# Performance work log

Hardware: AMD Instinct MI355X
Metric: run time of the kernel (lower is better)

The kernel has to match this reference:

```python
import jax, jax.numpy as jnp
import numpy as np

HEAD_SIZE = 128
NUM_EMBED = 1024
BLOCK_SIZE = 2048


def setup_inputs() -> dict:
    key = jax.random.key(0)
    kx, kk, kq, kv = jax.random.split(key, 4)
    x = jax.random.normal(kx, (4, BLOCK_SIZE, NUM_EMBED), dtype=jnp.float32)
    s = 1.0 / np.sqrt(NUM_EMBED)
    Wk = jax.random.normal(kk, (NUM_EMBED, HEAD_SIZE), dtype=jnp.float32) * s
    Wq = jax.random.normal(kq, (NUM_EMBED, HEAD_SIZE), dtype=jnp.float32) * s
    Wv = jax.random.normal(kv, (NUM_EMBED, HEAD_SIZE), dtype=jnp.float32) * s
    return {"x": x, "Wk": Wk, "Wq": Wq, "Wv": Wv}


def reference(x, Wk, Wq, Wv):
    # x: [B, T, C]; W*: [C, H]
    B, T, C = x.shape
    k = x @ Wk          # [B, T, H]
    q = x @ Wq          # [B, T, H]
    v = x @ Wv          # [B, T, H]
    scale = k.shape[-1] ** -0.5
    wei = jnp.einsum('bth,bsh->bts', q, k) * scale  # [B, T, T]
    causal = jnp.tril(jnp.ones((T, T), dtype=bool))
    wei = jnp.where(causal, wei, -jnp.inf)
    wei = jax.nn.softmax(wei, axis=-1)
    out = jnp.einsum('bts,bsh->bth', wei, v)        # [B, T, H]
    return out
```

## Files before the change

kernel.cpp:

```cpp
#include <hip/hip_runtime.h>
#include <hip/hip_bf16.h>
#include <math.h>

#define B_ 4
#define T_ 2048
#define C_ 1024
#define H_ 128
#define SCALE 0.088388347648318447f

typedef unsigned short u16;
typedef __bf16 bf16x8 __attribute__((ext_vector_type(8)));
typedef __bf16 bf16x4 __attribute__((ext_vector_type(4)));
typedef float  f32x4  __attribute__((ext_vector_type(4)));
typedef u16    u16x8  __attribute__((ext_vector_type(8)));
typedef u16    u16x4  __attribute__((ext_vector_type(4)));

#define PO_OFF  0u
#define ML_OFF  18874368u
#define WBT_OFF 19169280u
#define QB_OFF  19955712u
#define KB_OFF  22052864u
#define VT_OFF  24150016u

__device__ __forceinline__ u16 f2bf(float f) {
    __hip_bfloat16 h = __float2bfloat16(f);
    return __builtin_bit_cast(u16, h);
}
__device__ __forceinline__ float bf2f(u16 u) {
    unsigned v = (unsigned)u << 16;
    return __builtin_bit_cast(float, v);
}

__device__ __forceinline__ void load_lds16(const void* g, void* l) {
    __builtin_amdgcn_global_load_lds(
        (const __attribute__((address_space(1))) unsigned int*)g,
        (__attribute__((address_space(3))) unsigned int*)l, 16, 0, 0);
}

__global__ __launch_bounds__(256) void convert_w(const float* __restrict__ Wq,
                                                 const float* __restrict__ Wk,
                                                 const float* __restrict__ Wv,
                                                 u16* __restrict__ wbT) {
    const int id = blockIdx.x * 256 + threadIdx.x;
    const int s = id >> 17;
    const int r = id & 131071;
    const int k = r >> 7, n = r & 127;
    const float* W = (s == 0) ? Wq : (s == 1) ? Wk : Wv;
    float v = W[k * 128 + n];
    if (s == 0) v *= SCALE;
    wbT[(s << 17) + (n << 10) + k] = f2bf(v);
}

__global__ __launch_bounds__(256) void gemm_qkv(
    const float* __restrict__ x, const u16* __restrict__ wbT,
    u16* __restrict__ qb, u16* __restrict__ kb, u16* __restrict__ vT)
{
    __shared__ u16 xs[2][2048];
    __shared__ u16 ws[2][8192];

    const int tid = threadIdx.x;
    const int w = tid >> 6, lane = tid & 63, lg = lane >> 4, lr = lane & 15;
    const int wm = w >> 1, wn = w & 1;
    const int s = blockIdx.y;
    const int m0 = blockIdx.x * 32;
    const u16* wsrc = wbT + (s << 17);

    const int xrow = tid >> 3;
    const int xseg = tid & 7;
    const float* xbase = x + (size_t)(m0 + xrow) * C_ + xseg * 8;
    const unsigned xsw = ((unsigned)xrow & 7u) << 4;

    unsigned wro[4], wco[4];
#pragma unroll
    for (int i = 0; i < 4; ++i) {
        const unsigned o = (unsigned)(w * 4 + i) * 1024u + (unsigned)lane * 16u;
        const unsigned o2 = o ^ (((o >> 7) & 7u) << 4);
        wro[i] = o2 >> 7; wco[i] = (o2 & 127u) >> 1;
    }

    f32x4 acc[4] = {};

    {
        const float4 f0 = ((const float4*)xbase)[0], f1 = ((const float4*)xbase)[1];
#pragma unroll
        for (int i = 0; i < 4; ++i)
            load_lds16(wsrc + (size_t)wro[i] * C_ + wco[i], &ws[0][(w * 4 + i) * 512]);
        u16x8 pk;
        pk[0] = f2bf(f0.x); pk[1] = f2bf(f0.y); pk[2] = f2bf(f0.z); pk[3] = f2bf(f0.w);
        pk[4] = f2bf(f1.x); pk[5] = f2bf(f1.y); pk[6] = f2bf(f1.z); pk[7] = f2bf(f1.w);
        *(u16x8*)((char*)xs[0] + xrow * 128 + (((unsigned)xseg * 16) ^ xsw)) = pk;
    }
    __syncthreads();

    int buf = 0;
    for (int k0 = 0; k0 < C_; k0 += 64) {
        const bool pf = (k0 + 64 < C_);
        float4 g0, g1;
        if (pf) {
            const float* xn = xbase + k0 + 64;
            g0 = ((const float4*)xn)[0]; g1 = ((const float4*)xn)[1];
#pragma unroll
            for (int i = 0; i < 4; ++i)
                load_lds16(wsrc + (size_t)wro[i] * C_ + (k0 + 64) + wco[i],
                           &ws[buf ^ 1][(w * 4 + i) * 512]);
        }

        const int arow = wm * 16 + lr;
        const unsigned asw = ((unsigned)arow & 7u) << 4;
#pragma unroll
        for (int kc = 0; kc < 2; ++kc) {
            const unsigned kb_ = (unsigned)(kc * 64 + lg * 16);
            const bf16x8 af = *(const bf16x8*)((const char*)xs[buf] + arow * 128 + (kb_ ^ asw));
            bf16x8 bfr[4];
#pragma unroll
            for (int ni = 0; ni < 4; ++ni) {
                const int n = wn * 64 + ni * 16 + lr;
                bfr[ni] = *(const bf16x8*)((const char*)ws[buf] + n * 128 + (kb_ ^ (((unsigned)n & 7u) << 4)));
            }
#pragma unroll
            for (int ni = 0; ni < 4; ++ni)
                acc[ni] = __builtin_amdgcn_mfma_f32_16x16x32_bf16(af, bfr[ni], acc[ni], 0, 0, 0);
        }

        if (pf) {
            u16x8 pk;
            pk[0] = f2bf(g0.x); pk[1] = f2bf(g0.y); pk[2] = f2bf(g0.z); pk[3] = f2bf(g0.w);
            pk[4] = f2bf(g1.x); pk[5] = f2bf(g1.y); pk[6] = f2bf(g1.z); pk[7] = f2bf(g1.w);
            *(u16x8*)((char*)xs[buf ^ 1] + xrow * 128 + (((unsigned)xseg * 16) ^ xsw)) = pk;
        }
        __syncthreads();
        buf ^= 1;
    }

    if (s < 2) {
        u16* dst = (s == 0) ? qb : kb;
#pragma unroll
        for (int ni = 0; ni < 4; ++ni) {
            const int trow = m0 + wm * 16 + lg * 4;
            const int col = wn * 64 + ni * 16 + lr;
#pragma unroll
            for (int r = 0; r < 4; ++r)
                dst[(size_t)(trow + r) * H_ + col] = f2bf(acc[ni][r]);
        }
    } else {
#pragma unroll
        for (int ni = 0; ni < 4; ++ni) {
            const int trow = m0 + wm * 16 + lg * 4;
            const int bb = trow >> 11, t = trow & 2047;
            const int d = wn * 64 + ni * 16 + lr;
            u16x4 pk;
            pk[0] = f2bf(acc[ni][0]); pk[1] = f2bf(acc[ni][1]);
            pk[2] = f2bf(acc[ni][2]); pk[3] = f2bf(acc[ni][3]);
            *(u16x4*)&vT[((size_t)bb * 128 + d) * 2048 + t] = pk;
        }
    }
}

__global__ __launch_bounds__(256) void attn_split(
    const u16* __restrict__ qb, const u16* __restrict__ kb,
    const u16* __restrict__ vT, u16* __restrict__ po, float* __restrict__ ml)
{
    __shared__ u16 ks[2][4096];
    __shared__ u16 vs[2][128 * 36];

    const int jt = blockIdx.x, sp = blockIdx.y, b = blockIdx.z;
    const int kt0 = sp * 8;
    const int ktend_all = 2 * jt + 2;
    if (kt0 >= ktend_all) return;
    const int kt_end = min(kt0 + 8, ktend_all);

    const int tid = threadIdx.x;
    const int w = tid >> 6, lane = tid & 63, lg = lane >> 4, lr = lane & 15;
    const int qrow_base = jt * 64 + w * 16;

    const u16* kbB = kb + ((size_t)(b << 11)) * H_;
    const u16* vbB = vT + (size_t)b * 128 * 2048;

    unsigned krow[2], kcolb[2];
#pragma unroll
    for (int i = 0; i < 2; ++i) {
        const unsigned o_ = (unsigned)(w * 2 + i) * 1024u + (unsigned)lane * 16u;
        const unsigned o2 = o_ ^ (((o_ >> 8) & 7u) << 4);
        krow[i] = o2 >> 8; kcolb[i] = o2 & 255u;
    }
    int vd[2], vc[2];
#pragma unroll
    for (int i = 0; i < 2; ++i) {
        const int idx = i * 256 + tid;
        vd[i] = idx >> 2; vc[i] = idx & 3;
    }

    const u16* qp = qb + ((size_t)(b << 11) + qrow_base + lr) * H_;
    bf16x8 qf[4];
#pragma unroll
    for (int kc = 0; kc < 4; ++kc)
        qf[kc] = *(const bf16x8*)&qp[kc * 32 + lg * 8];

    u16x8 vr[2];
    {
        const u16* kbase = kbB + (size_t)kt0 * 32 * H_;
#pragma unroll
        for (int i = 0; i < 2; ++i)
            load_lds16((const char*)kbase + krow[i] * 256 + kcolb[i], &ks[0][(w * 2 + i) * 512]);
        const u16* vbase = vbB + (size_t)kt0 * 32;
#pragma unroll
        for (int i = 0; i < 2; ++i)
            vr[i] = *(const u16x8*)&vbase[(size_t)vd[i] * 2048 + vc[i] * 8];
#pragma unroll
        for (int i = 0; i < 2; ++i) {
            char* rb = (char*)vs[0] + vd[i] * 72 + (vc[i] & 2) * 4;
            *(u16x4*)(rb + ((2 * vc[i]) & 3) * 16)     = __builtin_shufflevector(vr[i], vr[i], 0, 1, 2, 3);
            *(u16x4*)(rb + ((2 * vc[i] + 1) & 3) * 16) = __builtin_shufflevector(vr[i], vr[i], 4, 5, 6, 7);
        }
    }
    __syncthreads();

    f32x4 o[8] = {};
    float m_run = -1e30f, l_run = 0.f;
    int cur = 0;

    for (int kt = kt0; kt < kt_end; ++kt) {
        const bool pf = (kt + 1 < kt_end);
        if (pf) {
            const u16* kbase = kbB + (size_t)(kt + 1) * 32 * H_;
#pragma unroll
            for (int i = 0; i < 2; ++i)
                load_lds16((const char*)kbase + krow[i] * 256 + kcolb[i],
                           &ks[cur ^ 1][(w * 2 + i) * 512]);
            const u16* vbase = vbB + (size_t)(kt + 1) * 32;
#pragma unroll
            for (int i = 0; i < 2; ++i)
                vr[i] = *(const u16x8*)&vbase[(size_t)vd[i] * 2048 + vc[i] * 8];
        }

        f32x4 s0 = {0.f, 0.f, 0.f, 0.f}, s1 = {0.f, 0.f, 0.f, 0.f};
        const unsigned swz = ((unsigned)lr & 7u) << 4;
#pragma unroll
        for (int kc = 0; kc < 4; ++kc) {
            const unsigned byte = ((unsigned)(kc * 64 + lg * 16)) ^ swz;
            const bf16x8 kf0 = *(const bf16x8*)((const char*)ks[cur] + lr * 256 + byte);
            const bf16x8 kf1 = *(const bf16x8*)((const char*)ks[cur] + lr * 256 + 4096 + byte);
            s0 = __builtin_amdgcn_mfma_f32_16x16x32_bf16(kf0, qf[kc], s0, 0, 0, 0);
            s1 = __builtin_amdgcn_mfma_f32_16x16x32_bf16(kf1, qf[kc], s1, 0, 0, 0);
        }

        if (kt * 32 + 31 > qrow_base) {
            const int qg = qrow_base + lr;
            const int kvb = kt * 32 + lg * 4;
#pragma unroll
            for (int r = 0; r < 4; ++r) {
                if (kvb + r > qg)      s0[r] = -INFINITY;
                if (kvb + 16 + r > qg) s1[r] = -INFINITY;
            }
        }

        float mt = fmaxf(fmaxf(fmaxf(s0[0], s0[1]), fmaxf(s0[2], s0[3])),
                         fmaxf(fmaxf(s1[0], s1[1]), fmaxf(s1[2], s1[3])));
        mt = fmaxf(mt, __shfl_xor(mt, 16));
        mt = fmaxf(mt, __shfl_xor(mt, 32));
        if (__any(mt > m_run + 8.f)) {
            const float mn = fmaxf(m_run, mt);
            const float f = __expf(m_run - mn);
            const float fb0 = __shfl(f, lg * 4 + 0);
            const float fb1 = __shfl(f, lg * 4 + 1);
            const float fb2 = __shfl(f, lg * 4 + 2);
            const float fb3 = __shfl(f, lg * 4 + 3);
#pragma unroll
            for (int ni = 0; ni < 8; ++ni) {
                o[ni][0] *= fb0; o[ni][1] *= fb1; o[ni][2] *= fb2; o[ni][3] *= fb3;
            }
            l_run *= f;
            m_run = mn;
        }
        const float p0 = __expf(s0[0] - m_run), p1 = __expf(s0[1] - m_run);
        const float p2 = __expf(s0[2] - m_run), p3 = __expf(s0[3] - m_run);
        const float p4 = __expf(s1[0] - m_run), p5 = __expf(s1[1] - m_run);
        const float p6 = __expf(s1[2] - m_run), p7 = __expf(s1[3] - m_run);
        float sum = ((p0 + p1) + (p2 + p3)) + ((p4 + p5) + (p6 + p7));
        sum += __shfl_xor(sum, 16);
        sum += __shfl_xor(sum, 32);
        l_run += sum;

        bf16x8 pa;
        pa[0] = (__bf16)p0; pa[1] = (__bf16)p1; pa[2] = (__bf16)p2; pa[3] = (__bf16)p3;
        pa[4] = (__bf16)p4; pa[5] = (__bf16)p5; pa[6] = (__bf16)p6; pa[7] = (__bf16)p7;

#pragma unroll
        for (int ni = 0; ni < 8; ++ni) {
            const bf16x8 vf = *(const bf16x8*)((const char*)vs[cur] + (ni * 16 + lr) * 72 + lg * 16);
            o[ni] = __builtin_amdgcn_mfma_f32_16x16x32_bf16(pa, vf, o[ni], 0, 0, 0);
        }

        if (pf) {
#pragma unroll
            for (int i = 0; i < 2; ++i) {
                char* rb = (char*)vs[cur ^ 1] + vd[i] * 72 + (vc[i] & 2) * 4;
                *(u16x4*)(rb + ((2 * vc[i]) & 3) * 16)     = __builtin_shufflevector(vr[i], vr[i], 0, 1, 2, 3);
                *(u16x4*)(rb + ((2 * vc[i] + 1) & 3) * 16) = __builtin_shufflevector(vr[i], vr[i], 4, 5, 6, 7);
            }
        }
        __syncthreads();
        cur ^= 1;
    }

    const int a = jt >> 2, b3 = jt & 3;
    const int slot = (a + 1) * (2 * a + b3) + sp;
    u16* pob = po + (size_t)(b * 144 + slot) * 64 * 128;
#pragma unroll
    for (int ni = 0; ni < 8; ++ni) {
        const int col = ni * 16 + lr;
#pragma unroll
        for (int rj = 0; rj < 4; ++rj)
            pob[(w * 16 + lg * 4 + rj) * 128 + col] = f2bf(o[ni][rj]);
    }
    if (lg == 0) {
        float* mlb = ml + (size_t)(b * 144 + slot) * 128;
        mlb[w * 16 + lr] = m_run;
        mlb[64 + w * 16 + lr] = l_run;
    }
}

__global__ __launch_bounds__(256) void attn_combine(
    const u16* __restrict__ po, const float* __restrict__ ml,
    float* __restrict__ out)
{
    const int rid = (blockIdx.x << 3) + (threadIdx.x >> 5);
    const int b = blockIdx.y;
    const int d4 = (threadIdx.x & 31) * 4;
    const int jt = rid >> 6, row = rid & 63;
    const int a = jt >> 2, b3 = jt & 3;
    const int slot0 = (a + 1) * (2 * a + b3);
    const int c = a + 1;

    float M = -INFINITY;
#pragma unroll
    for (int si = 0; si < 8; ++si)
        if (si < c) M = fmaxf(M, ml[(size_t)(b * 144 + slot0 + si) * 128 + row]);

    float L = 0.f;
    float a0 = 0.f, a1 = 0.f, a2 = 0.f, a3 = 0.f;
#pragma unroll
    for (int si = 0; si < 8; ++si) {
        if (si < c) {
            const float* mlb = ml + (size_t)(b * 144 + slot0 + si) * 128;
            const float wgt = __expf(mlb[row] - M);
            L += wgt * mlb[64 + row];
            const u16x4 t = *(const u16x4*)&po[((size_t)(b * 144 + slot0 + si) * 64 + row) * 128 + d4];
            a0 = fmaf(wgt, bf2f(t[0]), a0); a1 = fmaf(wgt, bf2f(t[1]), a1);
            a2 = fmaf(wgt, bf2f(t[2]), a2); a3 = fmaf(wgt, bf2f(t[3]), a3);
        }
    }
    const float inv = 1.f / L;
    *(float4*)&out[((size_t)(b << 11) + rid) * H_ + d4] =
        make_float4(a0 * inv, a1 * inv, a2 * inv, a3 * inv);
}

extern "C" void kernel_launch(void* const* d_in, const int* in_sizes, int n_in,
                              void* d_out, int out_size, void* d_ws, size_t ws_size,
                              hipStream_t stream) {
    const float* x  = (const float*)d_in[0];
    const float* Wk = (const float*)d_in[1];
    const float* Wq = (const float*)d_in[2];
    const float* Wv = (const float*)d_in[3];
    float* out = (float*)d_out;

    u16* po   = (u16*)((char*)d_ws + PO_OFF);
    float* ml = (float*)((char*)d_ws + ML_OFF);
    u16* wbT  = (u16*)((char*)d_ws + WBT_OFF);
    u16* qb   = (u16*)((char*)d_ws + QB_OFF);
    u16* kb   = (u16*)((char*)d_ws + KB_OFF);
    u16* vT   = (u16*)((char*)d_ws + VT_OFF);

    convert_w<<<1536, 256, 0, stream>>>(Wq, Wk, Wv, wbT);
    gemm_qkv<<<dim3(256, 3), 256, 0, stream>>>(x, wbT, qb, kb, vT);
    attn_split<<<dim3(32, 8, 4), 256, 0, stream>>>(qb, kb, vT, po, ml);
    attn_combine<<<dim3(256, 4), 256, 0, stream>>>(po, ml, out);
}
```

Before: 64.00 us.

## Pre-swizzle W, K, V into MFMA fragment order and drop LDS staging

Weights, K and V are now written in the exact per-lane MFMA fragment layout, so the QKV GEMM and the attention kernel read them straight from global memory into registers. This removes the LDS double-buffering and the barriers. The GEMM now loads the whole 32x1024 x tile into LDS once and reads W fragments directly from global. The aim is to cut LDS traffic and synchronization, at the cost of relying on cache and latency hiding for the direct global loads and of using more registers and a large LDS footprint in the GEMM, which lowers occupancy.

```diff
diff --git a/kernel.cpp b/kernel.cpp
--- a/kernel.cpp
+++ b/kernel.cpp
@@ -10,17 +10,16 @@
 
 typedef unsigned short u16;
 typedef __bf16 bf16x8 __attribute__((ext_vector_type(8)));
-typedef __bf16 bf16x4 __attribute__((ext_vector_type(4)));
 typedef float  f32x4  __attribute__((ext_vector_type(4)));
 typedef u16    u16x8  __attribute__((ext_vector_type(8)));
 typedef u16    u16x4  __attribute__((ext_vector_type(4)));
 
 #define PO_OFF  0u
 #define ML_OFF  18874368u
-#define WBT_OFF 19169280u
+#define WF_OFF  19169280u
 #define QB_OFF  19955712u
-#define KB_OFF  22052864u
-#define VT_OFF  24150016u
+#define KF_OFF  22052864u
+#define VF_OFF  24150016u
 
 __device__ __forceinline__ u16 f2bf(float f) {
     __hip_bfloat16 h = __float2bfloat16(f);
@@ -31,16 +30,10 @@
     return __builtin_bit_cast(float, v);
 }
 
-__device__ __forceinline__ void load_lds16(const void* g, void* l) {
-    __builtin_amdgcn_global_load_lds(
-        (const __attribute__((address_space(1))) unsigned int*)g,
-        (__attribute__((address_space(3))) unsigned int*)l, 16, 0, 0);
-}
-
 __global__ __launch_bounds__(256) void convert_w(const float* __restrict__ Wq,
                                                  const float* __restrict__ Wk,
                                                  const float* __restrict__ Wv,
-                                                 u16* __restrict__ wbT) {
+                                                 u16* __restrict__ wf) {
     const int id = blockIdx.x * 256 + threadIdx.x;
     const int s = id >> 17;
     const int r = id & 131071;
@@ -48,121 +41,116 @@
     const float* W = (s == 0) ? Wq : (s == 1) ? Wk : Wv;
     float v = W[k * 128 + n];
     if (s == 0) v *= SCALE;
-    wbT[(s << 17) + (n << 10) + k] = f2bf(v);
+    const int ntile = n >> 4, kstep = k >> 6, kc = (k >> 5) & 1;
+    const int lane = ((k >> 3) & 3) * 16 + (n & 15);
+    const int j = k & 7;
+    wf[((((size_t)(s * 8 + ntile) * 16 + kstep) * 2 + kc) * 64 + lane) * 8 + j] = f2bf(v);
 }
 
 __global__ __launch_bounds__(256) void gemm_qkv(
-    const float* __restrict__ x, const u16* __restrict__ wbT,
-    u16* __restrict__ qb, u16* __restrict__ kb, u16* __restrict__ vT)
+    const float* __restrict__ x, const u16* __restrict__ wf,
+    u16* __restrict__ qb, u16* __restrict__ kfr, u16* __restrict__ vfr)
 {
-    __shared__ u16 xs[2][2048];
-    __shared__ u16 ws[2][8192];
+    __shared__ u16 xs[32 * 1024];
 
     const int tid = threadIdx.x;
     const int w = tid >> 6, lane = tid & 63, lg = lane >> 4, lr = lane & 15;
-    const int wm = w >> 1, wn = w & 1;
     const int s = blockIdx.y;
     const int m0 = blockIdx.x * 32;
-    const u16* wsrc = wbT + (s << 17);
-
-    const int xrow = tid >> 3;
-    const int xseg = tid & 7;
-    const float* xbase = x + (size_t)(m0 + xrow) * C_ + xseg * 8;
-    const unsigned xsw = ((unsigned)xrow & 7u) << 4;
-
-    unsigned wro[4], wco[4];
-#pragma unroll
-    for (int i = 0; i < 4; ++i) {
-        const unsigned o = (unsigned)(w * 4 + i) * 1024u + (unsigned)lane * 16u;
-        const unsigned o2 = o ^ (((o >> 7) & 7u) << 4);
-        wro[i] = o2 >> 7; wco[i] = (o2 & 127u) >> 1;
-    }
-
-    f32x4 acc[4] = {};
 
     {
-        const float4 f0 = ((const float4*)xbase)[0], f1 = ((const float4*)xbase)[1];
-#pragma unroll
-        for (int i = 0; i < 4; ++i)
-            load_lds16(wsrc + (size_t)wro[i] * C_ + wco[i], &ws[0][(w * 4 + i) * 512]);
-        u16x8 pk;
-        pk[0] = f2bf(f0.x); pk[1] = f2bf(f0.y); pk[2] = f2bf(f0.z); pk[3] = f2bf(f0.w);
-        pk[4] = f2bf(f1.x); pk[5] = f2bf(f1.y); pk[6] = f2bf(f1.z); pk[7] = f2bf(f1.w);
-        *(u16x8*)((char*)xs[0] + xrow * 128 + (((unsigned)xseg * 16) ^ xsw)) = pk;
+        const float* xt = x + (size_t)m0 * C_;
+#pragma unroll
+        for (int i = 0; i < 32; ++i) {
+            const int fi = (i * 256 + tid) * 4;
+            const float4 f = *(const float4*)&xt[fi];
+            const int row = fi >> 10, col = fi & 1023;
+            u16x4 pk;
+            pk[0] = f2bf(f.x); pk[1] = f2bf(f.y); pk[2] = f2bf(f.z); pk[3] = f2bf(f.w);
+            *(u16x4*)((char*)xs + row * 2048 +
+                      (((unsigned)col * 2) ^ (((unsigned)row & 7u) << 4))) = pk;
+        }
     }
     __syncthreads();
 
-    int buf = 0;
-    for (int k0 = 0; k0 < C_; k0 += 64) {
-        const bool pf = (k0 + 64 < C_);
-        float4 g0, g1;
-        if (pf) {
-            const float* xn = xbase + k0 + 64;
-            g0 = ((const float4*)xn)[0]; g1 = ((const float4*)xn)[1];
-#pragma unroll
-            for (int i = 0; i < 4; ++i)
-                load_lds16(wsrc + (size_t)wro[i] * C_ + (k0 + 64) + wco[i],
-                           &ws[buf ^ 1][(w * 4 + i) * 512]);
-        }
-
-        const int arow = wm * 16 + lr;
-        const unsigned asw = ((unsigned)arow & 7u) << 4;
+    const u16* wbase = wf + (size_t)(s * 8) * 16 * 2 * 512 + (size_t)lane * 8;
+
+    f32x4 acc[2][2] = {};
+#pragma unroll 4
+    for (int kstep = 0; kstep < 16; ++kstep) {
 #pragma unroll
         for (int kc = 0; kc < 2; ++kc) {
-            const unsigned kb_ = (unsigned)(kc * 64 + lg * 16);
-            const bf16x8 af = *(const bf16x8*)((const char*)xs[buf] + arow * 128 + (kb_ ^ asw));
-            bf16x8 bfr[4];
-#pragma unroll
-            for (int ni = 0; ni < 4; ++ni) {
-                const int n = wn * 64 + ni * 16 + lr;
-                bfr[ni] = *(const bf16x8*)((const char*)ws[buf] + n * 128 + (kb_ ^ (((unsigned)n & 7u) << 4)));
-            }
-#pragma unroll
-            for (int ni = 0; ni < 4; ++ni)
-                acc[ni] = __builtin_amdgcn_mfma_f32_16x16x32_bf16(af, bfr[ni], acc[ni], 0, 0, 0);
-        }
-
-        if (pf) {
-            u16x8 pk;
-            pk[0] = f2bf(g0.x); pk[1] = f2bf(g0.y); pk[2] = f2bf(g0.z); pk[3] = f2bf(g0.w);
-            pk[4] = f2bf(g1.x); pk[5] = f2bf(g1.y); pk[6] = f2bf(g1.z); pk[7] = f2bf(g1.w);
-            *(u16x8*)((char*)xs[buf ^ 1] + xrow * 128 + (((unsigned)xseg * 16) ^ xsw)) = pk;
-        }
-        __syncthreads();
-        buf ^= 1;
-    }
-
-    if (s < 2) {
-        u16* dst = (s == 0) ? qb : kb;
-#pragma unroll
-        for (int ni = 0; ni < 4; ++ni) {
-            const int trow = m0 + wm * 16 + lg * 4;
-            const int col = wn * 64 + ni * 16 + lr;
-#pragma unroll
-            for (int r = 0; r < 4; ++r)
-                dst[(size_t)(trow + r) * H_ + col] = f2bf(acc[ni][r]);
-        }
+            const unsigned kbyte = (unsigned)(kstep * 128 + kc * 64 + lg * 16);
+            bf16x8 af[2];
+#pragma unroll
+            for (int mi = 0; mi < 2; ++mi) {
+                const int row = mi * 16 + lr;
+                af[mi] = *(const bf16x8*)((const char*)xs + row * 2048 +
+                                          (kbyte ^ (((unsigned)row & 7u) << 4)));
+            }
+#pragma unroll
+            for (int ni = 0; ni < 2; ++ni) {
+                const int ntile = w * 2 + ni;
+                const bf16x8 bfr = *(const bf16x8*)(wbase +
+                    (size_t)((ntile * 16 + kstep) * 2 + kc) * 512);
+#pragma unroll
+                for (int mi = 0; mi < 2; ++mi)
+                    acc[mi][ni] = __builtin_amdgcn_mfma_f32_16x16x32_bf16(
+                        af[mi], bfr, acc[mi][ni], 0, 0, 0);
+            }
+        }
+    }
+
+    if (s == 0) {
+#pragma unroll
+        for (int mi = 0; mi < 2; ++mi)
+#pragma unroll
+            for (int ni = 0; ni < 2; ++ni) {
+                const int trow = m0 + mi * 16 + lg * 4;
+                const int col = w * 32 + ni * 16 + lr;
+#pragma unroll
+                for (int r = 0; r < 4; ++r)
+                    qb[(size_t)(trow + r) * H_ + col] = f2bf(acc[mi][ni][r]);
+            }
+    } else if (s == 1) {
+#pragma unroll
+        for (int mi = 0; mi < 2; ++mi)
+#pragma unroll
+            for (int ni = 0; ni < 2; ++ni) {
+                const int d = w * 32 + ni * 16 + lr;
+                const int kc = d >> 5, lsub = ((d >> 3) & 3) << 4, j = d & 7;
+#pragma unroll
+                for (int r = 0; r < 4; ++r) {
+                    const int row = m0 + mi * 16 + lg * 4 + r;
+                    const int bb = row >> 11, tloc = (row >> 5) & 63;
+                    const int s2 = (row >> 4) & 1, rr = row & 15;
+                    kfr[(((size_t)((bb * 64 + tloc) * 2 + s2) * 4 + kc) * 64 +
+                         (rr | lsub)) * 8 + j] = f2bf(acc[mi][ni][r]);
+                }
+            }
     } else {
 #pragma unroll
-        for (int ni = 0; ni < 4; ++ni) {
-            const int trow = m0 + wm * 16 + lg * 4;
-            const int bb = trow >> 11, t = trow & 2047;
-            const int d = wn * 64 + ni * 16 + lr;
-            u16x4 pk;
-            pk[0] = f2bf(acc[ni][0]); pk[1] = f2bf(acc[ni][1]);
-            pk[2] = f2bf(acc[ni][2]); pk[3] = f2bf(acc[ni][3]);
-            *(u16x4*)&vT[((size_t)bb * 128 + d) * 2048 + t] = pk;
-        }
+        for (int mi = 0; mi < 2; ++mi)
+#pragma unroll
+            for (int ni = 0; ni < 2; ++ni) {
+                const int d = w * 32 + ni * 16 + lr;
+                const int nid = d >> 4;
+#pragma unroll
+                for (int r = 0; r < 4; ++r) {
+                    const int row = m0 + mi * 16 + lg * 4 + r;
+                    const int bb = row >> 11, tloc = (row >> 5) & 63, kv = row & 31;
+                    const int g = (kv & 15) >> 2, j = (kv >> 4) * 4 + (kv & 3);
+                    vfr[(((size_t)(bb * 64 + tloc) * 8 + nid) * 64 +
+                         ((g << 4) | (d & 15))) * 8 + j] = f2bf(acc[mi][ni][r]);
+                }
+            }
     }
 }
 
 __global__ __launch_bounds__(256) void attn_split(
-    const u16* __restrict__ qb, const u16* __restrict__ kb,
-    const u16* __restrict__ vT, u16* __restrict__ po, float* __restrict__ ml)
+    const u16* __restrict__ qb, const u16* __restrict__ kfr,
+    const u16* __restrict__ vfr, u16* __restrict__ po, float* __restrict__ ml)
 {
-    __shared__ u16 ks[2][4096];
-    __shared__ u16 vs[2][128 * 36];
-
     const int jt = blockIdx.x, sp = blockIdx.y, b = blockIdx.z;
     const int kt0 = sp * 8;
     const int ktend_all = 2 * jt + 2;
@@ -173,75 +161,37 @@
     const int w = tid >> 6, lane = tid & 63, lg = lane >> 4, lr = lane & 15;
     const int qrow_base = jt * 64 + w * 16;
 
-    const u16* kbB = kb + ((size_t)(b << 11)) * H_;
-    const u16* vbB = vT + (size_t)b * 128 * 2048;
-
-    unsigned krow[2], kcolb[2];
-#pragma unroll
-    for (int i = 0; i < 2; ++i) {
-        const unsigned o_ = (unsigned)(w * 2 + i) * 1024u + (unsigned)lane * 16u;
-        const unsigned o2 = o_ ^ (((o_ >> 8) & 7u) << 4);
-        krow[i] = o2 >> 8; kcolb[i] = o2 & 255u;
-    }
-    int vd[2], vc[2];
-#pragma unroll
-    for (int i = 0; i < 2; ++i) {
-        const int idx = i * 256 + tid;
-        vd[i] = idx >> 2; vc[i] = idx & 3;
-    }
-
     const u16* qp = qb + ((size_t)(b << 11) + qrow_base + lr) * H_;
     bf16x8 qf[4];
 #pragma unroll
     for (int kc = 0; kc < 4; ++kc)
         qf[kc] = *(const bf16x8*)&qp[kc * 32 + lg * 8];
 
-    u16x8 vr[2];
-    {
-        const u16* kbase = kbB + (size_t)kt0 * 32 * H_;
-#pragma unroll
-        for (int i = 0; i < 2; ++i)
-            load_lds16((const char*)kbase + krow[i] * 256 + kcolb[i], &ks[0][(w * 2 + i) * 512]);
-        const u16* vbase = vbB + (size_t)kt0 * 32;
-#pragma unroll
-        for (int i = 0; i < 2; ++i)
-            vr[i] = *(const u16x8*)&vbase[(size_t)vd[i] * 2048 + vc[i] * 8];
-#pragma unroll
-        for (int i = 0; i < 2; ++i) {
-            char* rb = (char*)vs[0] + vd[i] * 72 + (vc[i] & 2) * 4;
-            *(u16x4*)(rb + ((2 * vc[i]) & 3) * 16)     = __builtin_shufflevector(vr[i], vr[i], 0, 1, 2, 3);
-            *(u16x4*)(rb + ((2 * vc[i] + 1) & 3) * 16) = __builtin_shufflevector(vr[i], vr[i], 4, 5, 6, 7);
-        }
-    }
-    __syncthreads();
+    const u16* kfb = kfr + (size_t)(b * 64) * 4096 + (size_t)lane * 8;
+    const u16* vfb = vfr + (size_t)(b * 64) * 4096 + (size_t)lane * 8;
 
     f32x4 o[8] = {};
     float m_run = -1e30f, l_run = 0.f;
-    int cur = 0;
-
+
+#pragma unroll 2
     for (int kt = kt0; kt < kt_end; ++kt) {
-        const bool pf = (kt + 1 < kt_end);
-        if (pf) {
-            const u16* kbase = kbB + (size_t)(kt + 1) * 32 * H_;
-#pragma unroll
-            for (int i = 0; i < 2; ++i)
-                load_lds16((const char*)kbase + krow[i] * 256 + kcolb[i],
-                           &ks[cur ^ 1][(w * 2 + i) * 512]);
-            const u16* vbase = vbB + (size_t)(kt + 1) * 32;
-#pragma unroll
-            for (int i = 0; i < 2; ++i)
-                vr[i] = *(const u16x8*)&vbase[(size_t)vd[i] * 2048 + vc[i] * 8];
-        }
+        const u16* kft = kfb + (size_t)kt * 4096;
+        const u16* vft = vfb + (size_t)kt * 4096;
+        bf16x8 kf0[4], kf1[4], vf[8];
+#pragma unroll
+        for (int kc = 0; kc < 4; ++kc) {
+            kf0[kc] = *(const bf16x8*)(kft + kc * 512);
+            kf1[kc] = *(const bf16x8*)(kft + (4 + kc) * 512);
+        }
+#pragma unroll
+        for (int ni = 0; ni < 8; ++ni)
+            vf[ni] = *(const bf16x8*)(vft + ni * 512);
 
         f32x4 s0 = {0.f, 0.f, 0.f, 0.f}, s1 = {0.f, 0.f, 0.f, 0.f};
-        const unsigned swz = ((unsigned)lr & 7u) << 4;
 #pragma unroll
         for (int kc = 0; kc < 4; ++kc) {
-            const unsigned byte = ((unsigned)(kc * 64 + lg * 16)) ^ swz;
-            const bf16x8 kf0 = *(const bf16x8*)((const char*)ks[cur] + lr * 256 + byte);
-            const bf16x8 kf1 = *(const bf16x8*)((const char*)ks[cur] + lr * 256 + 4096 + byte);
-            s0 = __builtin_amdgcn_mfma_f32_16x16x32_bf16(kf0, qf[kc], s0, 0, 0, 0);
-            s1 = __builtin_amdgcn_mfma_f32_16x16x32_bf16(kf1, qf[kc], s1, 0, 0, 0);
+            s0 = __builtin_amdgcn_mfma_f32_16x16x32_bf16(kf0[kc], qf[kc], s0, 0, 0, 0);
+            s1 = __builtin_amdgcn_mfma_f32_16x16x32_bf16(kf1[kc], qf[kc], s1, 0, 0, 0);
         }
 
         if (kt * 32 + 31 > qrow_base) {
@@ -286,21 +236,8 @@
         pa[4] = (__bf16)p4; pa[5] = (__bf16)p5; pa[6] = (__bf16)p6; pa[7] = (__bf16)p7;
 
 #pragma unroll
-        for (int ni = 0; ni < 8; ++ni) {
-            const bf16x8 vf = *(const bf16x8*)((const char*)vs[cur] + (ni * 16 + lr) * 72 + lg * 16);
-            o[ni] = __builtin_amdgcn_mfma_f32_16x16x32_bf16(pa, vf, o[ni], 0, 0, 0);
-        }
-
-        if (pf) {
-#pragma unroll
-            for (int i = 0; i < 2; ++i) {
-                char* rb = (char*)vs[cur ^ 1] + vd[i] * 72 + (vc[i] & 2) * 4;
-                *(u16x4*)(rb + ((2 * vc[i]) & 3) * 16)     = __builtin_shufflevector(vr[i], vr[i], 0, 1, 2, 3);
-                *(u16x4*)(rb + ((2 * vc[i] + 1) & 3) * 16) = __builtin_shufflevector(vr[i], vr[i], 4, 5, 6, 7);
-            }
-        }
-        __syncthreads();
-        cur ^= 1;
+        for (int ni = 0; ni < 8; ++ni)
+            o[ni] = __builtin_amdgcn_mfma_f32_16x16x32_bf16(pa, vf[ni], o[ni], 0, 0, 0);
     }
 
     const int a = jt >> 2, b3 = jt & 3;
@@ -366,13 +303,13 @@
 
     u16* po   = (u16*)((char*)d_ws + PO_OFF);
     float* ml = (float*)((char*)d_ws + ML_OFF);
-    u16* wbT  = (u16*)((char*)d_ws + WBT_OFF);
+    u16* wf   = (u16*)((char*)d_ws + WF_OFF);
     u16* qb   = (u16*)((char*)d_ws + QB_OFF);
-    u16* kb   = (u16*)((char*)d_ws + KB_OFF);
-    u16* vT   = (u16*)((char*)d_ws + VT_OFF);
-
-    convert_w<<<1536, 256, 0, stream>>>(Wq, Wk, Wv, wbT);
-    gemm_qkv<<<dim3(256, 3), 256, 0, stream>>>(x, wbT, qb, kb, vT);
-    attn_split<<<dim3(32, 8, 4), 256, 0, stream>>>(qb, kb, vT, po, ml);
+    u16* kfr  = (u16*)((char*)d_ws + KF_OFF);
+    u16* vfr  = (u16*)((char*)d_ws + VF_OFF);
+
+    convert_w<<<1536, 256, 0, stream>>>(Wq, Wk, Wv, wf);
+    gemm_qkv<<<dim3(256, 3), 256, 0, stream>>>(x, wf, qb, kfr, vfr);
+    attn_split<<<dim3(32, 8, 4), 256, 0, stream>>>(qb, kfr, vfr, po, ml);
     attn_combine<<<dim3(256, 4), 256, 0, stream>>>(po, ml, out);
 }
```

Result: slower. 70.03 us (+9.4%).

## Fuse split-KV combine into attention kernel via last-block atomic counter

Applied to the files above, without the earlier changes.

Removes the separate combine kernel launch. Each split block atomically increments a per-(batch, query-tile) counter, and the last block to finish reads every split's partial output and max/sum stats to write the final normalized output. The counters are zeroed in the weight-conversion kernel. This trades a kernel launch and its tail for serialized combine work inside the last-finishing blocks, each thread holding 32 float accumulators that add register pressure.

```diff
diff --git a/kernel.cpp b/kernel.cpp
--- a/kernel.cpp
+++ b/kernel.cpp
@@ -10,7 +10,6 @@
 
 typedef unsigned short u16;
 typedef __bf16 bf16x8 __attribute__((ext_vector_type(8)));
-typedef __bf16 bf16x4 __attribute__((ext_vector_type(4)));
 typedef float  f32x4  __attribute__((ext_vector_type(4)));
 typedef u16    u16x8  __attribute__((ext_vector_type(8)));
 typedef u16    u16x4  __attribute__((ext_vector_type(4)));
@@ -21,6 +20,7 @@
 #define QB_OFF  19955712u
 #define KB_OFF  22052864u
 #define VT_OFF  24150016u
+#define CNT_OFF 26247168u
 
 __device__ __forceinline__ u16 f2bf(float f) {
     __hip_bfloat16 h = __float2bfloat16(f);
@@ -40,7 +40,9 @@
 __global__ __launch_bounds__(256) void convert_w(const float* __restrict__ Wq,
                                                  const float* __restrict__ Wk,
                                                  const float* __restrict__ Wv,
-                                                 u16* __restrict__ wbT) {
+                                                 u16* __restrict__ wbT,
+                                                 int* __restrict__ cnt) {
+    if (blockIdx.x == 0 && threadIdx.x < 128) cnt[threadIdx.x] = 0;
     const int id = blockIdx.x * 256 + threadIdx.x;
     const int s = id >> 17;
     const int r = id & 131071;
@@ -158,10 +160,12 @@
 
 __global__ __launch_bounds__(256) void attn_split(
     const u16* __restrict__ qb, const u16* __restrict__ kb,
-    const u16* __restrict__ vT, u16* __restrict__ po, float* __restrict__ ml)
+    const u16* __restrict__ vT, u16* __restrict__ po, float* __restrict__ ml,
+    int* __restrict__ cnt, float* __restrict__ out)
 {
     __shared__ u16 ks[2][4096];
     __shared__ u16 vs[2][128 * 36];
+    __shared__ int lastflag;
 
     const int jt = blockIdx.x, sp = blockIdx.y, b = blockIdx.z;
     const int kt0 = sp * 8;
@@ -304,7 +308,9 @@
     }
 
     const int a = jt >> 2, b3 = jt & 3;
-    const int slot = (a + 1) * (2 * a + b3) + sp;
+    const int slot0 = (a + 1) * (2 * a + b3);
+    const int slot = slot0 + sp;
+    const int c = a + 1;
     u16* pob = po + (size_t)(b * 144 + slot) * 64 * 128;
 #pragma unroll
     for (int ni = 0; ni < 8; ++ni) {
@@ -318,41 +324,47 @@
         mlb[w * 16 + lr] = m_run;
         mlb[64 + w * 16 + lr] = l_run;
     }
-}
-
-__global__ __launch_bounds__(256) void attn_combine(
-    const u16* __restrict__ po, const float* __restrict__ ml,
-    float* __restrict__ out)
-{
-    const int rid = (blockIdx.x << 3) + (threadIdx.x >> 5);
-    const int b = blockIdx.y;
-    const int d4 = (threadIdx.x & 31) * 4;
-    const int jt = rid >> 6, row = rid & 63;
-    const int a = jt >> 2, b3 = jt & 3;
-    const int slot0 = (a + 1) * (2 * a + b3);
-    const int c = a + 1;
-
+
+    __threadfence();
+    if (tid == 0) {
+        const int old = atomicAdd(&cnt[b * 32 + jt], 1);
+        lastflag = (old == c - 1);
+    }
+    __syncthreads();
+    if (!lastflag) return;
+    __threadfence();
+
+    const int rloc = tid >> 2;
+    const int seg = tid & 3;
     float M = -INFINITY;
-#pragma unroll
-    for (int si = 0; si < 8; ++si)
-        if (si < c) M = fmaxf(M, ml[(size_t)(b * 144 + slot0 + si) * 128 + row]);
-
+    for (int si = 0; si < c; ++si)
+        M = fmaxf(M, ml[(size_t)(b * 144 + slot0 + si) * 128 + rloc]);
     float L = 0.f;
-    float a0 = 0.f, a1 = 0.f, a2 = 0.f, a3 = 0.f;
-#pragma unroll
-    for (int si = 0; si < 8; ++si) {
-        if (si < c) {
-            const float* mlb = ml + (size_t)(b * 144 + slot0 + si) * 128;
-            const float wgt = __expf(mlb[row] - M);
-            L += wgt * mlb[64 + row];
-            const u16x4 t = *(const u16x4*)&po[((size_t)(b * 144 + slot0 + si) * 64 + row) * 128 + d4];
-            a0 = fmaf(wgt, bf2f(t[0]), a0); a1 = fmaf(wgt, bf2f(t[1]), a1);
-            a2 = fmaf(wgt, bf2f(t[2]), a2); a3 = fmaf(wgt, bf2f(t[3]), a3);
+    float accf[32];
+#pragma unroll
+    for (int i = 0; i < 32; ++i) accf[i] = 0.f;
+    for (int si = 0; si < c; ++si) {
+        const float* mlb = ml + (size_t)(b * 144 + slot0 + si) * 128;
+        const float wgt = __expf(mlb[rloc] - M);
+        L += wgt * mlb[64 + rloc];
+        const u16* pr = po + ((size_t)(b * 144 + slot0 + si) * 64 + rloc) * 128 + seg * 32;
+#pragma unroll
+        for (int i = 0; i < 4; ++i) {
+            const u16x8 t = *(const u16x8*)&pr[i * 8];
+#pragma unroll
+            for (int jj = 0; jj < 8; ++jj)
+                accf[i * 8 + jj] = fmaf(wgt, bf2f(t[jj]), accf[i * 8 + jj]);
         }
     }
     const float inv = 1.f / L;
-    *(float4*)&out[((size_t)(b << 11) + rid) * H_ + d4] =
-        make_float4(a0 * inv, a1 * inv, a2 * inv, a3 * inv);
+    float* ob = out + ((size_t)(b << 11) + jt * 64 + rloc) * H_ + seg * 32;
+#pragma unroll
+    for (int i = 0; i < 8; ++i) {
+        f32x4 v4;
+        v4[0] = accf[i * 4 + 0] * inv; v4[1] = accf[i * 4 + 1] * inv;
+        v4[2] = accf[i * 4 + 2] * inv; v4[3] = accf[i * 4 + 3] * inv;
+        *(f32x4*)&ob[i * 4] = v4;
+    }
 }
 
 extern "C" void kernel_launch(void* const* d_in, const int* in_sizes, int n_in,
@@ -370,9 +382,9 @@
     u16* qb   = (u16*)((char*)d_ws + QB_OFF);
     u16* kb   = (u16*)((char*)d_ws + KB_OFF);
     u16* vT   = (u16*)((char*)d_ws + VT_OFF);
-
-    convert_w<<<1536, 256, 0, stream>>>(Wq, Wk, Wv, wbT);
+    int* cnt  = (int*)((char*)d_ws + CNT_OFF);
+
+    convert_w<<<1536, 256, 0, stream>>>(Wq, Wk, Wv, wbT, cnt);
     gemm_qkv<<<dim3(256, 3), 256, 0, stream>>>(x, wbT, qb, kb, vT);
-    attn_split<<<dim3(32, 8, 4), 256, 0, stream>>>(qb, kb, vT, po, ml);
-    attn_combine<<<dim3(256, 4), 256, 0, stream>>>(po, ml, out);
-}
+    attn_split<<<dim3(32, 8, 4), 256, 0, stream>>>(qb, kb, vT, po, ml, cnt, out);
+}
```

Result: slower. 156.4 us (+144.4%).

## Pre-swizzle weights into MFMA fragment layout and stage full x tile in LDS

Applied to the files above, without the earlier changes.

The weight conversion now writes W in a per-lane MFMA fragment order, so the GEMM loads B fragments directly from global memory (through cache) with no LDS staging. The full 32x1024 x tile is converted to bf16 into LDS once, which removes the per-k-step double buffer and its barriers. Each wave now owns 32 output columns with a 2x2 tile of accumulators. The cost is a 64KB LDS footprint per block, which lowers occupancy, and a serialized upfront load with no overlap against compute.

```diff
diff --git a/kernel.cpp b/kernel.cpp
--- a/kernel.cpp
+++ b/kernel.cpp
@@ -10,14 +10,13 @@
 
 typedef unsigned short u16;
 typedef __bf16 bf16x8 __attribute__((ext_vector_type(8)));
-typedef __bf16 bf16x4 __attribute__((ext_vector_type(4)));
 typedef float  f32x4  __attribute__((ext_vector_type(4)));
 typedef u16    u16x8  __attribute__((ext_vector_type(8)));
 typedef u16    u16x4  __attribute__((ext_vector_type(4)));
 
 #define PO_OFF  0u
 #define ML_OFF  18874368u
-#define WBT_OFF 19169280u
+#define WF_OFF  19169280u
 #define QB_OFF  19955712u
 #define KB_OFF  22052864u
 #define VT_OFF  24150016u
@@ -40,7 +39,7 @@
 __global__ __launch_bounds__(256) void convert_w(const float* __restrict__ Wq,
                                                  const float* __restrict__ Wk,
                                                  const float* __restrict__ Wv,
-                                                 u16* __restrict__ wbT) {
+                                                 u16* __restrict__ wf) {
     const int id = blockIdx.x * 256 + threadIdx.x;
     const int s = id >> 17;
     const int r = id & 131071;
@@ -48,111 +47,91 @@
     const float* W = (s == 0) ? Wq : (s == 1) ? Wk : Wv;
     float v = W[k * 128 + n];
     if (s == 0) v *= SCALE;
-    wbT[(s << 17) + (n << 10) + k] = f2bf(v);
+    const int ntile = n >> 4, kstep = k >> 6, kc = (k >> 5) & 1;
+    const int lane = ((k >> 3) & 3) * 16 + (n & 15);
+    const int j = k & 7;
+    wf[((((size_t)(s * 8 + ntile) * 16 + kstep) * 2 + kc) * 64 + lane) * 8 + j] = f2bf(v);
 }
 
 __global__ __launch_bounds__(256) void gemm_qkv(
-    const float* __restrict__ x, const u16* __restrict__ wbT,
+    const float* __restrict__ x, const u16* __restrict__ wf,
     u16* __restrict__ qb, u16* __restrict__ kb, u16* __restrict__ vT)
 {
-    __shared__ u16 xs[2][2048];
-    __shared__ u16 ws[2][8192];
+    __shared__ u16 xs[32 * 1024];
 
     const int tid = threadIdx.x;
     const int w = tid >> 6, lane = tid & 63, lg = lane >> 4, lr = lane & 15;
-    const int wm = w >> 1, wn = w & 1;
     const int s = blockIdx.y;
     const int m0 = blockIdx.x * 32;
-    const u16* wsrc = wbT + (s << 17);
-
-    const int xrow = tid >> 3;
-    const int xseg = tid & 7;
-    const float* xbase = x + (size_t)(m0 + xrow) * C_ + xseg * 8;
-    const unsigned xsw = ((unsigned)xrow & 7u) << 4;
-
-    unsigned wro[4], wco[4];
-#pragma unroll
-    for (int i = 0; i < 4; ++i) {
-        const unsigned o = (unsigned)(w * 4 + i) * 1024u + (unsigned)lane * 16u;
-        const unsigned o2 = o ^ (((o >> 7) & 7u) << 4);
-        wro[i] = o2 >> 7; wco[i] = (o2 & 127u) >> 1;
-    }
-
-    f32x4 acc[4] = {};
 
     {
-        const float4 f0 = ((const float4*)xbase)[0], f1 = ((const float4*)xbase)[1];
-#pragma unroll
-        for (int i = 0; i < 4; ++i)
-            load_lds16(wsrc + (size_t)wro[i] * C_ + wco[i], &ws[0][(w * 4 + i) * 512]);
-        u16x8 pk;
-        pk[0] = f2bf(f0.x); pk[1] = f2bf(f0.y); pk[2] = f2bf(f0.z); pk[3] = f2bf(f0.w);
-        pk[4] = f2bf(f1.x); pk[5] = f2bf(f1.y); pk[6] = f2bf(f1.z); pk[7] = f2bf(f1.w);
-        *(u16x8*)((char*)xs[0] + xrow * 128 + (((unsigned)xseg * 16) ^ xsw)) = pk;
+        const float* xt = x + (size_t)m0 * C_;
+#pragma unroll
+        for (int i = 0; i < 32; ++i) {
+            const int fi = (i * 256 + tid) * 4;
+            const float4 f = *(const float4*)&xt[fi];
+            const int row = fi >> 10, col = fi & 1023;
+            u16x4 pk;
+            pk[0] = f2bf(f.x); pk[1] = f2bf(f.y); pk[2] = f2bf(f.z); pk[3] = f2bf(f.w);
+            *(u16x4*)((char*)xs + row * 2048 +
+                      (((unsigned)col * 2) ^ (((unsigned)row & 7u) << 4))) = pk;
+        }
     }
     __syncthreads();
 
-    int buf = 0;
-    for (int k0 = 0; k0 < C_; k0 += 64) {
-        const bool pf = (k0 + 64 < C_);
-        float4 g0, g1;
-        if (pf) {
-            const float* xn = xbase + k0 + 64;
-            g0 = ((const float4*)xn)[0]; g1 = ((const float4*)xn)[1];
-#pragma unroll
-            for (int i = 0; i < 4; ++i)
-                load_lds16(wsrc + (size_t)wro[i] * C_ + (k0 + 64) + wco[i],
-                           &ws[buf ^ 1][(w * 4 + i) * 512]);
-        }
-
-        const int arow = wm * 16 + lr;
-        const unsigned asw = ((unsigned)arow & 7u) << 4;
+    const u16* wbase = wf + (size_t)(s * 8) * 16 * 2 * 512 + (size_t)lane * 8;
+
+    f32x4 acc[2][2] = {};
+#pragma unroll 4
+    for (int kstep = 0; kstep < 16; ++kstep) {
 #pragma unroll
         for (int kc = 0; kc < 2; ++kc) {
-            const unsigned kb_ = (unsigned)(kc * 64 + lg * 16);
-            const bf16x8 af = *(const bf16x8*)((const char*)xs[buf] + arow * 128 + (kb_ ^ asw));
-            bf16x8 bfr[4];
-#pragma unroll
-            for (int ni = 0; ni < 4; ++ni) {
-                const int n = wn * 64 + ni * 16 + lr;
-                bfr[ni] = *(const bf16x8*)((const char*)ws[buf] + n * 128 + (kb_ ^ (((unsigned)n & 7u) << 4)));
-            }
-#pragma unroll
-            for (int ni = 0; ni < 4; ++ni)
-                acc[ni] = __builtin_amdgcn_mfma_f32_16x16x32_bf16(af, bfr[ni], acc[ni], 0, 0, 0);
-        }
-
-        if (pf) {
-            u16x8 pk;
-            pk[0] = f2bf(g0.x); pk[1] = f2bf(g0.y); pk[2] = f2bf(g0.z); pk[3] = f2bf(g0.w);
-            pk[4] = f2bf(g1.x); pk[5] = f2bf(g1.y); pk[6] = f2bf(g1.z); pk[7] = f2bf(g1.w);
-            *(u16x8*)((char*)xs[buf ^ 1] + xrow * 128 + (((unsigned)xseg * 16) ^ xsw)) = pk;
-        }
-        __syncthreads();
-        buf ^= 1;
+            const unsigned kbyte = (unsigned)(kstep * 128 + kc * 64 + lg * 16);
+            bf16x8 af[2];
+#pragma unroll
+            for (int mi = 0; mi < 2; ++mi) {
+                const int row = mi * 16 + lr;
+                af[mi] = *(const bf16x8*)((const char*)xs + row * 2048 +
+                                          (kbyte ^ (((unsigned)row & 7u) << 4)));
+            }
+#pragma unroll
+            for (int ni = 0; ni < 2; ++ni) {
+                const int ntile = w * 2 + ni;
+                const bf16x8 bfr = *(const bf16x8*)(wbase +
+                    (size_t)((ntile * 16 + kstep) * 2 + kc) * 512);
+#pragma unroll
+                for (int mi = 0; mi < 2; ++mi)
+                    acc[mi][ni] = __builtin_amdgcn_mfma_f32_16x16x32_bf16(
+                        af[mi], bfr, acc[mi][ni], 0, 0, 0);
+            }
+        }
     }
 
     if (s < 2) {
         u16* dst = (s == 0) ? qb : kb;
 #pragma unroll
-        for (int ni = 0; ni < 4; ++ni) {
-            const int trow = m0 + wm * 16 + lg * 4;
-            const int col = wn * 64 + ni * 16 + lr;
-#pragma unroll
-            for (int r = 0; r < 4; ++r)
-                dst[(size_t)(trow + r) * H_ + col] = f2bf(acc[ni][r]);
-        }
+        for (int mi = 0; mi < 2; ++mi)
+#pragma unroll
+            for (int ni = 0; ni < 2; ++ni) {
+                const int trow = m0 + mi * 16 + lg * 4;
+                const int col = w * 32 + ni * 16 + lr;
+#pragma unroll
+                for (int r = 0; r < 4; ++r)
+                    dst[(size_t)(trow + r) * H_ + col] = f2bf(acc[mi][ni][r]);
+            }
     } else {
 #pragma unroll
-        for (int ni = 0; ni < 4; ++ni) {
-            const int trow = m0 + wm * 16 + lg * 4;
-            const int bb = trow >> 11, t = trow & 2047;
-            const int d = wn * 64 + ni * 16 + lr;
-            u16x4 pk;
-            pk[0] = f2bf(acc[ni][0]); pk[1] = f2bf(acc[ni][1]);
-            pk[2] = f2bf(acc[ni][2]); pk[3] = f2bf(acc[ni][3]);
-            *(u16x4*)&vT[((size_t)bb * 128 + d) * 2048 + t] = pk;
-        }
+        for (int mi = 0; mi < 2; ++mi)
+#pragma unroll
+            for (int ni = 0; ni < 2; ++ni) {
+                const int trow = m0 + mi * 16 + lg * 4;
+                const int bb = trow >> 11, t = trow & 2047;
+                const int d = w * 32 + ni * 16 + lr;
+                u16x4 pk;
+                pk[0] = f2bf(acc[mi][ni][0]); pk[1] = f2bf(acc[mi][ni][1]);
+                pk[2] = f2bf(acc[mi][ni][2]); pk[3] = f2bf(acc[mi][ni][3]);
+                *(u16x4*)&vT[((size_t)bb * 128 + d) * 2048 + t] = pk;
+            }
     }
 }
 
@@ -366,13 +345,13 @@
 
     u16* po   = (u16*)((char*)d_ws + PO_OFF);
     float* ml = (float*)((char*)d_ws + ML_OFF);
-    u16* wbT  = (u16*)((char*)d_ws + WBT_OFF);
+    u16* wf   = (u16*)((char*)d_ws + WF_OFF);
     u16* qb   = (u16*)((char*)d_ws + QB_OFF);
     u16* kb   = (u16*)((char*)d_ws + KB_OFF);
     u16* vT   = (u16*)((char*)d_ws + VT_OFF);
 
-    convert_w<<<1536, 256, 0, stream>>>(Wq, Wk, Wv, wbT);
-    gemm_qkv<<<dim3(256, 3), 256, 0, stream>>>(x, wbT, qb, kb, vT);
+    convert_w<<<1536, 256, 0, stream>>>(Wq, Wk, Wv, wf);
+    gemm_qkv<<<dim3(256, 3), 256, 0, stream>>>(x, wf, qb, kb, vT);
     attn_split<<<dim3(32, 8, 4), 256, 0, stream>>>(qb, kb, vT, po, ml);
     attn_combine<<<dim3(256, 4), 256, 0, stream>>>(po, ml, out);
 }
```

Result: slower. 68.85 us (+7.6%).
